# Kernel optimization log

Hardware: AMD Instinct MI355X
Metric: run time of the kernel (lower is better)

Reference implementation:

```python
import jax, jax.numpy as jnp
import numpy as np

N_NODES = 50000
N_EDGES = 800000
N_GRAPHS = 64
HID = 128
FEAT = 64
OUT = 32
N_LAYERS = 3
DECAY = 0.9
THRESH = 0.1


def setup_inputs() -> dict:
    key = jax.random.key(0)
    ks = jax.random.split(key, 24)
    s = 0.05
    inp = {
        "x": jax.random.normal(ks[0], (N_NODES, FEAT), jnp.float32),
        "edge_attr": jax.random.normal(ks[1], (N_EDGES, 1), jnp.float32),
        "initial_importance": jax.random.uniform(ks[2], (N_NODES, 1), jnp.float32),
        "imp_proj_W": jax.random.normal(ks[3], (1, HID), jnp.float32) * s,
        "imp_proj_b": jnp.zeros((HID,), jnp.float32),
        "init_W": jax.random.normal(ks[4], (FEAT + HID, HID), jnp.float32) * s,
        "init_b": jnp.zeros((HID,), jnp.float32),
        "msg_W": jax.random.normal(ks[5], (N_LAYERS, HID, HID), jnp.float32) * s,
        "msg_b": jnp.zeros((N_LAYERS, HID), jnp.float32),
        "upd_W": jax.random.normal(ks[6], (N_LAYERS, 2 * HID, HID), jnp.float32) * s,
        "upd_b": jnp.zeros((N_LAYERS, HID), jnp.float32),
        "gate_W": jax.random.normal(ks[7], (N_LAYERS, HID + 1, HID), jnp.float32) * s,
        "gate_b": jnp.zeros((N_LAYERS, HID), jnp.float32),
        "prop_W": jax.random.normal(ks[8], (N_LAYERS, HID, 1), jnp.float32) * s,
        "prop_b": jnp.zeros((N_LAYERS, 1), jnp.float32),
        "norm_w": jnp.ones((N_LAYERS, HID), jnp.float32),
        "norm_b": jnp.zeros((N_LAYERS, HID), jnp.float32),
        "norm_a": jnp.ones((N_LAYERS, HID), jnp.float32),
        "final_W": jax.random.normal(ks[9], (HID, OUT), jnp.float32) * s,
        "final_b": jnp.zeros((OUT,), jnp.float32),
        "edge_index": jax.random.randint(ks[10], (2, N_EDGES), 0, N_NODES, jnp.int32),
        # evenly spread sorted graph ids -> every graph non-empty
        "batch": (jnp.arange(N_NODES, dtype=jnp.int32) * N_GRAPHS) // N_NODES,
    }
    return inp


def _normalize_importance(imp, batch):
    # per-graph min/max normalization, fused segment reductions
    mn = jax.ops.segment_min(imp, batch, num_segments=N_GRAPHS)[batch]
    mx = jax.ops.segment_max(imp, batch, num_segments=N_GRAPHS)[batch]
    return (imp - mn) / (mx - mn + 1e-8)


def _graph_norm(x, batch, counts, w, b, a):
    # PyG GraphNorm: y = w * (x - a*mean) / sqrt(var(x - a*mean) + eps) + b
    mean = jax.ops.segment_sum(x, batch, num_segments=N_GRAPHS) / counts
    out = x - a * mean[batch]
    var = jax.ops.segment_sum(out * out, batch, num_segments=N_GRAPHS) / counts
    std = jnp.sqrt(var + 1e-5)
    return w * out / std[batch] + b


def _forward(x, edge_attr, initial_importance, imp_proj_W, imp_proj_b, init_W,
             init_b, msg_W, msg_b, upd_W, upd_b, gate_W, gate_b, prop_W, prop_b,
             norm_w, norm_b, norm_a, final_W, final_b, edge_index, batch):
    src, dst = edge_index[0], edge_index[1]
    counts = jax.ops.segment_sum(jnp.ones((N_NODES, 1), x.dtype), batch,
                                 num_segments=N_GRAPHS)  # [G,1]

    imp0 = initial_importance[:, 0]                       # [N]
    importance = _normalize_importance(imp0, batch)       # [N]
    imp_emb = importance[:, None] @ imp_proj_W + imp_proj_b  # [N,H]
    h = jnp.concatenate([x, imp_emb], axis=-1) @ init_W + init_b  # [N,H]

    for l in range(N_LAYERS):
        # MPNN: gather -> linear -> scatter-add -> update
        msg = h[src] @ msg_W[l] + msg_b[l]                # [E,H]
        aggr = jax.ops.segment_sum(msg, dst, num_segments=N_NODES)  # [N,H]
        conv = jnp.concatenate([h, aggr], axis=-1) @ upd_W[l] + upd_b[l]
        # importance gating
        gate_in = jnp.concatenate([conv, importance[:, None]], axis=-1)
        gate = jax.nn.sigmoid(gate_in @ gate_W[l] + gate_b[l])
        out = gate * conv + (1.0 - gate) * h
        prop = out @ prop_W[l] + prop_b[l]                # [N,1]
        # norm + relu (dropout p=0 in eval)
        h = jax.nn.relu(_graph_norm(out, batch, counts, norm_w[l], norm_b[l], norm_a[l]))
        # importance update
        imp = DECAY * importance + (1.0 - DECAY) * prop[:, 0]
        imp = _normalize_importance(imp, batch)
        imp = jnp.where(imp < THRESH, 0.0, imp)
        importance = _normalize_importance(imp, batch)

    h = h @ final_W + final_b                             # [N,OUT]
    logits = jax.ops.segment_sum(h, batch, num_segments=N_GRAPHS) / counts  # [G,OUT]
    final_importance = _normalize_importance(imp0 + importance, batch)
    return logits, final_importance[:, None]


def reference(x, edge_attr, initial_importance, imp_proj_W, imp_proj_b, init_W,
              init_b, msg_W, msg_b, upd_W, upd_b, gate_W, gate_b, prop_W, prop_b,
              norm_w, norm_b, norm_a, final_W, final_b, edge_index, batch):
    return _forward(x, edge_attr, initial_importance, imp_proj_W, imp_proj_b,
                    init_W, init_b, msg_W, msg_b, upd_W, upd_b, gate_W, gate_b,
                    prop_W, prop_b, norm_w, norm_b, norm_a, final_W, final_b,
                    edge_index, batch)
```

## Files before the change

kernel.cpp:

```cpp
#include <hip/hip_runtime.h>
#include <cstdint>

#define NN 50000
#define NE 800000
#define NG 64
#define HD 128
#define FT 64
#define NLAYERS 3
#define MB 32
#define NBLK 1563

__global__ void k_gbounds(const int* __restrict__ batch, int* __restrict__ gstart){
    int i = blockIdx.x*blockDim.x + threadIdx.x;
    if (i >= NN) return;
    int g = batch[i];
    if (i == 0){ for (int q = 0; q <= g; ++q) gstart[q] = 0; }
    else { int gp = batch[i-1]; for (int q = gp+1; q <= g; ++q) gstart[q] = i; }
    if (i == NN-1){ for (int q = g+1; q <= NG; ++q) gstart[q] = NN; }
}

__device__ __forceinline__ void block_minmax(float lmn, float lmx, float* red,
                                             float& omn, float& omx){
    #pragma unroll
    for (int off = 32; off > 0; off >>= 1){
        lmn = fminf(lmn, __shfl_xor(lmn, off));
        lmx = fmaxf(lmx, __shfl_xor(lmx, off));
    }
    int wave = threadIdx.x >> 6;
    if ((threadIdx.x & 63) == 0){ red[wave] = lmn; red[4+wave] = lmx; }
    __syncthreads();
    omn = fminf(fminf(red[0], red[1]), fminf(red[2], red[3]));
    omx = fmaxf(fmaxf(red[4], red[5]), fmaxf(red[6], red[7]));
    __syncthreads();
}

__global__ __launch_bounds__(256) void k_norm_graph(
    const float* __restrict__ va, const int* __restrict__ gstart,
    float* __restrict__ out)
{
    __shared__ float sv[1024];
    __shared__ float red[8];
    int g = blockIdx.x;
    int s = gstart[g], n = gstart[g+1] - s;
    int tid = threadIdx.x;
    float lmn = 3.4e38f, lmx = -3.4e38f;
    for (int i = tid; i < n; i += 256){
        float v = va[s+i];
        sv[i] = v;
        lmn = fminf(lmn, v); lmx = fmaxf(lmx, v);
    }
    float lo, hi;
    block_minmax(lmn, lmx, red, lo, hi);
    float inv = 1.f/(hi - lo + 1e-8f);
    for (int i = tid; i < n; i += 256) out[s+i] = (sv[i] - lo)*inv;
}

__global__ void k_fold_init(const float* __restrict__ pW, const float* __restrict__ pb,
                            const float* __restrict__ iW, const float* __restrict__ ib,
                            float* __restrict__ W0, float* __restrict__ b0){
    int j = threadIdx.x;
    for (int k = 0; k < FT; ++k) W0[k*HD + j] = iW[k*HD + j];
    float w2 = 0.f, b2 = 0.f;
    for (int k = 0; k < HD; ++k){
        float w = iW[(FT + k)*HD + j];
        w2 += pW[k]*w;
        b2 += pb[k]*w;
    }
    W0[FT*HD + j] = w2;
    b0[j] = ib[j] + b2;
}

__global__ void k_fold_layer(const float* __restrict__ msgW, const float* __restrict__ updW,
                             const float* __restrict__ msgb,
                             float* __restrict__ WfA, float* __restrict__ bcvA){
    int l = blockIdx.y;
    const float* mW  = msgW + (size_t)l*HD*HD;
    const float* uW  = updW + (size_t)l*2*HD*HD;
    const float* mb  = msgb + (size_t)l*HD;
    float* Wf  = WfA  + (size_t)l*2*HD*HD;
    float* bcv = bcvA + (size_t)l*HD;
    int j = threadIdx.x;
    int r = blockIdx.x;
    if (r < HD){
        Wf[(size_t)r*HD + j] = uW[(size_t)r*HD + j];
    } else if (r < 2*HD){
        int rr = r - HD;
        const float* uWbot = uW + (size_t)HD*HD;
        float acc = 0.f;
        for (int k = 0; k < HD; ++k)
            acc = fmaf(mW[(size_t)rr*HD + k], uWbot[(size_t)k*HD + j], acc);
        Wf[(size_t)r*HD + j] = acc;
    } else {
        const float* uWbot = uW + (size_t)HD*HD;
        float acc = 0.f;
        for (int k = 0; k < HD; ++k)
            acc = fmaf(mb[k], uWbot[(size_t)k*HD + j], acc);
        bcv[j] = acc;
    }
}

__global__ __launch_bounds__(256) void k_init(
    const float* __restrict__ x, const float* __restrict__ imp,
    const float* __restrict__ W0, const float* __restrict__ b0v,
    float* __restrict__ h)
{
    __shared__ float lds[MB][FT];
    __shared__ float scs[MB];
    int base = blockIdx.x*MB, tid = threadIdx.x;
    #pragma unroll
    for (int i = 0; i < 2; ++i){
        int fidx = i*256 + tid;
        int t = fidx >> 4, c = fidx & 15;
        float4 v = {0.f,0.f,0.f,0.f};
        if (base + t < NN) v = *(const float4*)&x[(size_t)(base+t)*FT + c*4];
        *(float4*)&lds[t][c*4] = v;
    }
    if (tid < MB) scs[tid] = (base+tid < NN) ? imp[base+tid] : 0.f;
    __syncthreads();

    const int cg = tid & 31, rg = tid >> 5;
    const int c0 = cg*4, r0 = rg*4;
    const float4 wl4 = *(const float4*)&W0[(size_t)FT*HD + c0];
    const float4 b4  = *(const float4*)&b0v[c0];
    float acc[4][4];
    #pragma unroll
    for (int r = 0; r < 4; ++r){
        float s = scs[r0+r];
        acc[r][0] = fmaf(s, wl4.x, b4.x); acc[r][1] = fmaf(s, wl4.y, b4.y);
        acc[r][2] = fmaf(s, wl4.z, b4.z); acc[r][3] = fmaf(s, wl4.w, b4.w);
    }
    for (int k4 = 0; k4 < 16; ++k4){
        const float4 w0 = *(const float4*)&W0[(size_t)(k4*4+0)*HD + c0];
        const float4 w1 = *(const float4*)&W0[(size_t)(k4*4+1)*HD + c0];
        const float4 w2 = *(const float4*)&W0[(size_t)(k4*4+2)*HD + c0];
        const float4 w3 = *(const float4*)&W0[(size_t)(k4*4+3)*HD + c0];
        #pragma unroll
        for (int r = 0; r < 4; ++r){
            const float4 a = *(const float4*)&lds[r0+r][k4*4];
            acc[r][0]=fmaf(a.x,w0.x,fmaf(a.y,w1.x,fmaf(a.z,w2.x,fmaf(a.w,w3.x,acc[r][0]))));
            acc[r][1]=fmaf(a.x,w0.y,fmaf(a.y,w1.y,fmaf(a.z,w2.y,fmaf(a.w,w3.y,acc[r][1]))));
            acc[r][2]=fmaf(a.x,w0.z,fmaf(a.y,w1.z,fmaf(a.z,w2.z,fmaf(a.w,w3.z,acc[r][2]))));
            acc[r][3]=fmaf(a.x,w0.w,fmaf(a.y,w1.w,fmaf(a.z,w2.w,fmaf(a.w,w3.w,acc[r][3]))));
        }
    }
    #pragma unroll
    for (int r = 0; r < 4; ++r)
        if (base + r0 + r < NN)
            *(float4*)&h[(size_t)(base+r0+r)*HD + c0] =
                make_float4(acc[r][0], acc[r][1], acc[r][2], acc[r][3]);
}

__global__ __launch_bounds__(256) void k_layer(
    const float* __restrict__ h, const float* __restrict__ aggr,
    const float* __restrict__ imp, const int* __restrict__ deg,
    const float* __restrict__ Wf, const float* __restrict__ bcv,
    const float* __restrict__ ub,
    const float* __restrict__ gW, const float* __restrict__ gb,
    const float* __restrict__ prW, const float* __restrict__ prb,
    float* __restrict__ outbuf, float* __restrict__ ta)
{
    __shared__ float lds[MB][256];
    __shared__ float clds[MB][HD];
    __shared__ float scs[MB];
    __shared__ float dgs[MB];
    __shared__ float red[8][4];
    const int base = blockIdx.x*MB, tid = threadIdx.x;

    #pragma unroll
    for (int i = 0; i < 8; ++i){
        int fidx = i*256 + tid;
        int t = fidx >> 6, c = fidx & 63;
        float4 v = {0.f,0.f,0.f,0.f};
        if (base + t < NN){
            const float* srcp = (c < 32) ? &h[(size_t)(base+t)*HD + c*4]
                                         : &aggr[(size_t)(base+t)*HD + (c-32)*4];
            v = *(const float4*)srcp;
        }
        *(float4*)&lds[t][c*4] = v;
    }
    if (tid < MB) scs[tid] = (base+tid < NN) ? imp[base+tid] : 0.f;
    else if (tid < 2*MB){
        int t = tid - MB;
        dgs[t] = (base+t < NN) ? (float)deg[base+t] : 0.f;
    }
    __syncthreads();

    const int cg = tid & 31, rg = tid >> 5;
    const int c0 = cg*4, r0 = rg*4;

    const float4 bc4 = *(const float4*)&bcv[c0];
    const float4 ub4 = *(const float4*)&ub[c0];
    float acc[4][4];
    #pragma unroll
    for (int r = 0; r < 4; ++r){
        float d = dgs[r0+r];
        acc[r][0] = fmaf(d, bc4.x, ub4.x); acc[r][1] = fmaf(d, bc4.y, ub4.y);
        acc[r][2] = fmaf(d, bc4.z, ub4.z); acc[r][3] = fmaf(d, bc4.w, ub4.w);
    }
    for (int k4 = 0; k4 < 64; ++k4){
        const float4 w0 = *(const float4*)&Wf[(size_t)(k4*4+0)*HD + c0];
        const float4 w1 = *(const float4*)&Wf[(size_t)(k4*4+1)*HD + c0];
        const float4 w2 = *(const float4*)&Wf[(size_t)(k4*4+2)*HD + c0];
        const float4 w3 = *(const float4*)&Wf[(size_t)(k4*4+3)*HD + c0];
        #pragma unroll
        for (int r = 0; r < 4; ++r){
            const float4 a = *(const float4*)&lds[r0+r][k4*4];
            acc[r][0]=fmaf(a.x,w0.x,fmaf(a.y,w1.x,fmaf(a.z,w2.x,fmaf(a.w,w3.x,acc[r][0]))));
            acc[r][1]=fmaf(a.x,w0.y,fmaf(a.y,w1.y,fmaf(a.z,w2.y,fmaf(a.w,w3.y,acc[r][1]))));
            acc[r][2]=fmaf(a.x,w0.z,fmaf(a.y,w1.z,fmaf(a.z,w2.z,fmaf(a.w,w3.z,acc[r][2]))));
            acc[r][3]=fmaf(a.x,w0.w,fmaf(a.y,w1.w,fmaf(a.z,w2.w,fmaf(a.w,w3.w,acc[r][3]))));
        }
    }
    #pragma unroll
    for (int r = 0; r < 4; ++r)
        *(float4*)&clds[r0+r][c0] = make_float4(acc[r][0],acc[r][1],acc[r][2],acc[r][3]);
    __syncthreads();

    const float4 gwl = *(const float4*)&gW[(size_t)HD*HD + c0];
    const float4 gb4 = *(const float4*)&gb[c0];
    float z[4][4];
    #pragma unroll
    for (int r = 0; r < 4; ++r){
        float s = scs[r0+r];
        z[r][0] = fmaf(s, gwl.x, gb4.x); z[r][1] = fmaf(s, gwl.y, gb4.y);
        z[r][2] = fmaf(s, gwl.z, gb4.z); z[r][3] = fmaf(s, gwl.w, gb4.w);
    }
    for (int k4 = 0; k4 < 32; ++k4){
        const float4 w0 = *(const float4*)&gW[(size_t)(k4*4+0)*HD + c0];
        const float4 w1 = *(const float4*)&gW[(size_t)(k4*4+1)*HD + c0];
        const float4 w2 = *(const float4*)&gW[(size_t)(k4*4+2)*HD + c0];
        const float4 w3 = *(const float4*)&gW[(size_t)(k4*4+3)*HD + c0];
        #pragma unroll
        for (int r = 0; r < 4; ++r){
            const float4 a = *(const float4*)&clds[r0+r][k4*4];
            z[r][0]=fmaf(a.x,w0.x,fmaf(a.y,w1.x,fmaf(a.z,w2.x,fmaf(a.w,w3.x,z[r][0]))));
            z[r][1]=fmaf(a.x,w0.y,fmaf(a.y,w1.y,fmaf(a.z,w2.y,fmaf(a.w,w3.y,z[r][1]))));
            z[r][2]=fmaf(a.x,w0.z,fmaf(a.y,w1.z,fmaf(a.z,w2.z,fmaf(a.w,w3.z,z[r][2]))));
            z[r][3]=fmaf(a.x,w0.w,fmaf(a.y,w1.w,fmaf(a.z,w2.w,fmaf(a.w,w3.w,z[r][3]))));
        }
    }

    const float4 pr4 = *(const float4*)&prW[c0];
    float psum[4];
    #pragma unroll
    for (int r = 0; r < 4; ++r){
        const float4 hv = *(const float4*)&lds[r0+r][c0];
        float g0 = 1.f/(1.f + expf(-z[r][0]));
        float g1 = 1.f/(1.f + expf(-z[r][1]));
        float g2 = 1.f/(1.f + expf(-z[r][2]));
        float g3 = 1.f/(1.f + expf(-z[r][3]));
        float o0 = g0*acc[r][0] + (1.f-g0)*hv.x;
        float o1 = g1*acc[r][1] + (1.f-g1)*hv.y;
        float o2 = g2*acc[r][2] + (1.f-g2)*hv.z;
        float o3 = g3*acc[r][3] + (1.f-g3)*hv.w;
        if (base + r0 + r < NN)
            *(float4*)&outbuf[(size_t)(base+r0+r)*HD + c0] = make_float4(o0,o1,o2,o3);
        psum[r] = o0*pr4.x + o1*pr4.y + o2*pr4.z + o3*pr4.w;
    }
    #pragma unroll
    for (int r = 0; r < 4; ++r){
        float v = psum[r];
        #pragma unroll
        for (int off = 16; off > 0; off >>= 1) v += __shfl_xor(v, off);
        if (cg == 0) red[rg][r] = v;
    }
    __syncthreads();
    if (tid < MB && base + tid < NN)
        ta[base+tid] = 0.9f*scs[tid] + 0.1f*(red[tid>>2][tid&3] + prb[0]);
}

__global__ void k_deg(const int* __restrict__ dst, int* deg){
    int e = blockIdx.x*blockDim.x + threadIdx.x;
    if (e < NE) atomicAdd(&deg[dst[e]], 1);
}

__global__ __launch_bounds__(1024) void k_scan(const int* __restrict__ deg,
                                               int* __restrict__ rowstart){
    __shared__ int wtot[16];
    __shared__ int woff[16];
    __shared__ int carry;
    int tid = threadIdx.x, lane = tid & 63, wv = tid >> 6;
    if (tid == 0) carry = 0;
    __syncthreads();
    for (int base = 0; base < NN; base += 1024){
        int i = base + tid;
        int v = (i < NN) ? deg[i] : 0;
        int x = v;
        #pragma unroll
        for (int off = 1; off < 64; off <<= 1){
            int y = __shfl_up(x, off);
            if (lane >= off) x += y;
        }
        if (lane == 63) wtot[wv] = x;
        __syncthreads();
        if (tid == 0){
            int a = carry;
            for (int w2 = 0; w2 < 16; ++w2){ woff[w2] = a; a += wtot[w2]; }
            carry = a;
        }
        __syncthreads();
        if (i < NN) rowstart[i] = woff[wv] + x - v;
    }
    __syncthreads();
    if (tid == 0) rowstart[NN] = carry;
}

__global__ void k_copy_int(const int* __restrict__ a, int* __restrict__ b, int n){
    int i = blockIdx.x*blockDim.x + threadIdx.x;
    if (i < n) b[i] = a[i];
}

__global__ void k_fill(const int* __restrict__ src, const int* __restrict__ dst,
                       int* cursor, int* __restrict__ csr){
    int e = blockIdx.x*blockDim.x + threadIdx.x;
    if (e < NE){
        int d = dst[e];
        int p = atomicAdd(&cursor[d], 1);
        csr[p] = src[e];
    }
}

__global__ __launch_bounds__(256) void k_aggregate(
    const float* __restrict__ hm, const int* __restrict__ rowstart,
    const int* __restrict__ csr, float* __restrict__ aggr)
{
    int node = blockIdx.x*8 + (threadIdx.x >> 5);
    int lane = threadIdx.x & 31;
    float4 a0 = {0.f,0.f,0.f,0.f}, a1 = a0, a2 = a0, a3 = a0;
    float4 a4 = a0, a5 = a0, a6 = a0, a7 = a0;
    int e0 = rowstart[node], e1 = rowstart[node+1];
    int e = e0;
    for (; e + 7 < e1; e += 8){
        int s0 = csr[e],   s1 = csr[e+1], s2 = csr[e+2], s3 = csr[e+3];
        int s4 = csr[e+4], s5 = csr[e+5], s6 = csr[e+6], s7 = csr[e+7];
        const float4 v0 = *(const float4*)&hm[(size_t)s0*HD + lane*4];
        const float4 v1 = *(const float4*)&hm[(size_t)s1*HD + lane*4];
        const float4 v2 = *(const float4*)&hm[(size_t)s2*HD + lane*4];
        const float4 v3 = *(const float4*)&hm[(size_t)s3*HD + lane*4];
        const float4 v4 = *(const float4*)&hm[(size_t)s4*HD + lane*4];
        const float4 v5 = *(const float4*)&hm[(size_t)s5*HD + lane*4];
        const float4 v6 = *(const float4*)&hm[(size_t)s6*HD + lane*4];
        const float4 v7 = *(const float4*)&hm[(size_t)s7*HD + lane*4];
        a0.x += v0.x; a0.y += v0.y; a0.z += v0.z; a0.w += v0.w;
        a1.x += v1.x; a1.y += v1.y; a1.z += v1.z; a1.w += v1.w;
        a2.x += v2.x; a2.y += v2.y; a2.z += v2.z; a2.w += v2.w;
        a3.x += v3.x; a3.y += v3.y; a3.z += v3.z; a3.w += v3.w;
        a4.x += v4.x; a4.y += v4.y; a4.z += v4.z; a4.w += v4.w;
        a5.x += v5.x; a5.y += v5.y; a5.z += v5.z; a5.w += v5.w;
        a6.x += v6.x; a6.y += v6.y; a6.z += v6.z; a6.w += v6.w;
        a7.x += v7.x; a7.y += v7.y; a7.z += v7.z; a7.w += v7.w;
    }
    for (; e + 3 < e1; e += 4){
        int s0 = csr[e], s1 = csr[e+1], s2 = csr[e+2], s3 = csr[e+3];
        const float4 v0 = *(const float4*)&hm[(size_t)s0*HD + lane*4];
        const float4 v1 = *(const float4*)&hm[(size_t)s1*HD + lane*4];
        const float4 v2 = *(const float4*)&hm[(size_t)s2*HD + lane*4];
        const float4 v3 = *(const float4*)&hm[(size_t)s3*HD + lane*4];
        a0.x += v0.x; a0.y += v0.y; a0.z += v0.z; a0.w += v0.w;
        a1.x += v1.x; a1.y += v1.y; a1.z += v1.z; a1.w += v1.w;
        a2.x += v2.x; a2.y += v2.y; a2.z += v2.z; a2.w += v2.w;
        a3.x += v3.x; a3.y += v3.y; a3.z += v3.z; a3.w += v3.w;
    }
    for (; e < e1; ++e){
        int s0 = csr[e];
        const float4 v0 = *(const float4*)&hm[(size_t)s0*HD + lane*4];
        a0.x += v0.x; a0.y += v0.y; a0.z += v0.z; a0.w += v0.w;
    }
    a0.x += a1.x; a0.y += a1.y; a0.z += a1.z; a0.w += a1.w;
    a2.x += a3.x; a2.y += a3.y; a2.z += a3.z; a2.w += a3.w;
    a4.x += a5.x; a4.y += a5.y; a4.z += a5.z; a4.w += a5.w;
    a6.x += a7.x; a6.y += a7.y; a6.z += a7.z; a6.w += a7.w;
    a0.x += a2.x; a0.y += a2.y; a0.z += a2.z; a0.w += a2.w;
    a4.x += a6.x; a4.y += a6.y; a4.z += a6.z; a4.w += a6.w;
    a0.x += a4.x; a0.y += a4.y; a0.z += a4.z; a0.w += a4.w;
    *(float4*)&aggr[(size_t)node*HD + lane*4] = a0;
}

__global__ __launch_bounds__(256) void k_gnorm(
    const float* __restrict__ v, const int* __restrict__ gstart,
    const float* __restrict__ nw, const float* __restrict__ nb,
    const float* __restrict__ na, float* __restrict__ hout,
    const float* __restrict__ tsrc, float* __restrict__ tdst)
{
    int g = blockIdx.x;
    int part = blockIdx.y;
    int s = gstart[g], n = gstart[g+1] - s;
    int tid = threadIdx.x;

    if (part == 4){
        __shared__ float sv[1024];
        __shared__ float red[8];
        float lmn = 3.4e38f, lmx = -3.4e38f;
        for (int i = tid; i < n; i += 256){
            float val = tsrc[s+i]; sv[i] = val;
            lmn = fminf(lmn, val); lmx = fmaxf(lmx, val);
        }
        float lo, hi;
        block_minmax(lmn, lmx, red, lo, hi);
        float inv = 1.f/(hi - lo + 1e-8f);
        lmn = 3.4e38f; lmx = -3.4e38f;
        for (int i = tid; i < n; i += 256){
            float t2 = (sv[i] - lo)*inv;
            if (t2 < 0.1f) t2 = 0.f;
            sv[i] = t2;
            lmn = fminf(lmn, t2); lmx = fmaxf(lmx, t2);
        }
        float lo2, hi2;
        block_minmax(lmn, lmx, red, lo2, hi2);
        float inv2 = 1.f/(hi2 - lo2 + 1e-8f);
        for (int i = tid; i < n; i += 256) tdst[s+i] = (sv[i] - lo2)*inv2;
        return;
    }

    __shared__ float4 rs1[32][8];
    __shared__ float4 rs2[32][8];
    __shared__ float amv[32], scv[32], nbv[32];
    int rg = tid >> 3, c4l = tid & 7;
    size_t coff = (size_t)part*32 + c4l*4;
    float4 s1 = {0.f,0.f,0.f,0.f}, s2 = {0.f,0.f,0.f,0.f};
    for (int i = rg; i < n; i += 32){
        const float4 vv = *(const float4*)&v[(size_t)(s+i)*HD + coff];
        s1.x += vv.x; s1.y += vv.y; s1.z += vv.z; s1.w += vv.w;
        s2.x += vv.x*vv.x; s2.y += vv.y*vv.y; s2.z += vv.z*vv.z; s2.w += vv.w*vv.w;
    }
    rs1[rg][c4l] = s1; rs2[rg][c4l] = s2;
    __syncthreads();
    if (tid < 8){
        float4 t1 = {0.f,0.f,0.f,0.f}, t2 = {0.f,0.f,0.f,0.f};
        for (int r = 0; r < 32; ++r){
            float4 a = rs1[r][tid]; float4 b = rs2[r][tid];
            t1.x += a.x; t1.y += a.y; t1.z += a.z; t1.w += a.w;
            t2.x += b.x; t2.y += b.y; t2.z += b.z; t2.w += b.w;
        }
        float fn = (float)n;
        float S1[4] = {t1.x,t1.y,t1.z,t1.w};
        float S2[4] = {t2.x,t2.y,t2.z,t2.w};
        #pragma unroll
        for (int e = 0; e < 4; ++e){
            int j = part*32 + tid*4 + e;
            float m = S1[e]/fn;
            float aj = na[j];
            float var = S2[e]/fn - (2.f*aj - aj*aj)*m*m;
            float stdv = sqrtf(var + 1e-5f);
            amv[tid*4+e] = aj*m;
            scv[tid*4+e] = nw[j]/stdv;
            nbv[tid*4+e] = nb[j];
        }
    }
    __syncthreads();
    const float4 am4 = *(const float4*)&amv[c4l*4];
    const float4 sc4 = *(const float4*)&scv[c4l*4];
    const float4 nb4 = *(const float4*)&nbv[c4l*4];
    for (int i = rg; i < n; i += 32){
        const float4 vv = *(const float4*)&v[(size_t)(s+i)*HD + coff];
        float4 r;
        r.x = fmaxf((vv.x - am4.x)*sc4.x + nb4.x, 0.f);
        r.y = fmaxf((vv.y - am4.y)*sc4.y + nb4.y, 0.f);
        r.z = fmaxf((vv.z - am4.z)*sc4.z + nb4.z, 0.f);
        r.w = fmaxf((vv.w - am4.w)*sc4.w + nb4.w, 0.f);
        *(float4*)&hout[(size_t)(s+i)*HD + coff] = r;
    }
}

__global__ __launch_bounds__(1024) void k_logits(
    const float* __restrict__ h, const int* __restrict__ gstart,
    const float* __restrict__ fW, const float* __restrict__ fb,
    const float* __restrict__ imp0, const float* __restrict__ impf,
    float* __restrict__ outp)
{
    __shared__ float4 rs1[32][32];
    __shared__ float gsum[HD];
    __shared__ float redn[32];
    int g = blockIdx.x;
    int s = gstart[g], n = gstart[g+1] - s;
    int tid = threadIdx.x;
    int c4 = tid & 31, rg = tid >> 5;
    float4 s1 = {0.f,0.f,0.f,0.f};
    for (int i = rg; i < n; i += 32){
        const float4 vv = *(const float4*)&h[(size_t)(s+i)*HD + c4*4];
        s1.x += vv.x; s1.y += vv.y; s1.z += vv.z; s1.w += vv.w;
    }
    rs1[rg][c4] = s1;
    __syncthreads();
    if (tid < 32){
        float4 t1 = {0.f,0.f,0.f,0.f};
        for (int r = 0; r < 32; ++r){
            float4 a = rs1[r][tid];
            t1.x += a.x; t1.y += a.y; t1.z += a.z; t1.w += a.w;
        }
        gsum[tid*4+0] = t1.x; gsum[tid*4+1] = t1.y;
        gsum[tid*4+2] = t1.z; gsum[tid*4+3] = t1.w;
    }
    __syncthreads();
    if (tid < 32){
        int o = tid;
        float acc = 0.f;
        for (int k = 0; k < HD; ++k) acc = fmaf(gsum[k], fW[k*32 + o], acc);
        outp[g*32 + o] = acc/(float)n + fb[o];
    }
    float val = 0.f;
    bool has = (tid < n);
    float lmn = 3.4e38f, lmx = -3.4e38f;
    if (has){ val = imp0[s+tid] + impf[s+tid]; lmn = val; lmx = val; }
    #pragma unroll
    for (int off = 32; off > 0; off >>= 1){
        lmn = fminf(lmn, __shfl_xor(lmn, off));
        lmx = fmaxf(lmx, __shfl_xor(lmx, off));
    }
    int wv = tid >> 6, lane = tid & 63;
    if (lane == 0){ redn[wv] = lmn; redn[16+wv] = lmx; }
    __syncthreads();
    float lo = redn[0], hi = redn[16];
    for (int r2 = 1; r2 < 16; ++r2){
        lo = fminf(lo, redn[r2]); hi = fmaxf(hi, redn[16+r2]);
    }
    if (has) outp[NG*32 + s + tid] = (val - lo)/(hi - lo + 1e-8f);
}

extern "C" void kernel_launch(void* const* d_in, const int* in_sizes, int n_in,
                              void* d_out, int out_size, void* d_ws, size_t ws_size,
                              hipStream_t stream){
    const float* x    = (const float*)d_in[0];
    const float* imp0 = (const float*)d_in[2];
    const float* pW   = (const float*)d_in[3];
    const float* pb   = (const float*)d_in[4];
    const float* iW   = (const float*)d_in[5];
    const float* ib   = (const float*)d_in[6];
    const float* msgW = (const float*)d_in[7];
    const float* msgb = (const float*)d_in[8];
    const float* updW = (const float*)d_in[9];
    const float* updb = (const float*)d_in[10];
    const float* gWt  = (const float*)d_in[11];
    const float* gb   = (const float*)d_in[12];
    const float* prW  = (const float*)d_in[13];
    const float* prb  = (const float*)d_in[14];
    const float* nw   = (const float*)d_in[15];
    const float* nb   = (const float*)d_in[16];
    const float* na   = (const float*)d_in[17];
    const float* fW   = (const float*)d_in[18];
    const float* fb   = (const float*)d_in[19];
    const int* eidx   = (const int*)d_in[20];
    const int* batch  = (const int*)d_in[21];
    const int* esrc = eidx;
    const int* edst = eidx + NE;
    float* outp = (float*)d_out;

    char* w = (char*)d_ws;
    size_t off = 0;
    auto alloc = [&](size_t bytes)->char*{
        char* p = w + off;
        off += (bytes + 255) & ~(size_t)255;
        return p;
    };
    float* h     = (float*)alloc((size_t)NN*HD*4);
    float* aggB  = (float*)alloc((size_t)NN*HD*4);
    float* outA  = (float*)alloc((size_t)NN*HD*4);
    float* ta    = (float*)alloc((size_t)NN*4);
    float* imp   = (float*)alloc((size_t)NN*4);
    float* W0    = (float*)alloc((size_t)(FT+1)*HD*4);
    float* b0    = (float*)alloc((size_t)HD*4);
    float* Wf    = (float*)alloc((size_t)NLAYERS*2*HD*HD*4);
    float* bcv   = (float*)alloc((size_t)NLAYERS*HD*4);
    int* gstart  = (int*)alloc((size_t)(NG+1)*4);
    int* deg     = (int*)alloc((size_t)NN*4);
    int* rowst   = (int*)alloc((size_t)(NN+1)*4);
    int* cursor  = (int*)alloc((size_t)NN*4);
    int* csr     = (int*)alloc((size_t)NE*4);

    k_gbounds<<<196, 256, 0, stream>>>(batch, gstart);

    hipMemsetAsync(deg, 0, NN*4, stream);
    k_deg<<<3125, 256, 0, stream>>>(edst, deg);
    k_scan<<<1, 1024, 0, stream>>>(deg, rowst);
    k_copy_int<<<196, 256, 0, stream>>>(rowst, cursor, NN);
    k_fill<<<3125, 256, 0, stream>>>(esrc, edst, cursor, csr);

    k_fold_init<<<1, 128, 0, stream>>>(pW, pb, iW, ib, W0, b0);
    k_fold_layer<<<dim3(257, NLAYERS), 128, 0, stream>>>(msgW, updW, msgb, Wf, bcv);

    k_norm_graph<<<NG, 256, 0, stream>>>(imp0, gstart, imp);
    k_init<<<NBLK, 256, 0, stream>>>(x, imp, W0, b0, h);

    for (int l = 0; l < NLAYERS; ++l){
        k_aggregate<<<6250, 256, 0, stream>>>(h, rowst, csr, aggB);
        k_layer<<<NBLK, 256, 0, stream>>>(
            h, aggB, imp, deg,
            Wf + (size_t)l*2*HD*HD, bcv + (size_t)l*HD,
            updb + (size_t)l*HD, gWt + (size_t)l*(HD+1)*HD, gb + (size_t)l*HD,
            prW + (size_t)l*HD, prb + l, outA, ta);
        k_gnorm<<<dim3(NG,5), 256, 0, stream>>>(outA, gstart,
            nw + (size_t)l*HD, nb + (size_t)l*HD, na + (size_t)l*HD, h, ta, imp);
    }

    k_logits<<<NG, 1024, 0, stream>>>(h, gstart, fW, fb, imp0, imp, outp);
}
```

Measured before the change: 705.7 us.

## Split aggregation into feature slices with 4 lanes per node; trim layer LDS

The gather aggregation now splits the 128-wide feature row into 8 slices of 16 floats, one slice per block, with 4 threads per node and 64 nodes per block. Each block touches only a 64-byte column band of the node table, which is meant to shrink the working set each block pulls through cache. In exchange every block rereads the CSR row indices, about 8 times more index traffic overall. k_layer drops its separate clds buffer and reuses the upper half of lds after an extra barrier to cut LDS use, and it sets launch_bounds occupancy to 4 and adds unroll-4 pragmas on the GEMM loops.

```diff
diff --git a/kernel.cpp b/kernel.cpp
--- a/kernel.cpp
+++ b/kernel.cpp
@@ -9,6 +9,8 @@
 #define NLAYERS 3
 #define MB 32
 #define NBLK 1563
+#define AGN 64
+#define AGB (8*((NN + AGN - 1)/AGN))
 
 __global__ void k_gbounds(const int* __restrict__ batch, int* __restrict__ gstart){
     int i = blockIdx.x*blockDim.x + threadIdx.x;
@@ -129,6 +131,7 @@
         acc[r][0] = fmaf(s, wl4.x, b4.x); acc[r][1] = fmaf(s, wl4.y, b4.y);
         acc[r][2] = fmaf(s, wl4.z, b4.z); acc[r][3] = fmaf(s, wl4.w, b4.w);
     }
+    #pragma unroll 4
     for (int k4 = 0; k4 < 16; ++k4){
         const float4 w0 = *(const float4*)&W0[(size_t)(k4*4+0)*HD + c0];
         const float4 w1 = *(const float4*)&W0[(size_t)(k4*4+1)*HD + c0];
@@ -150,7 +153,7 @@
                 make_float4(acc[r][0], acc[r][1], acc[r][2], acc[r][3]);
 }
 
-__global__ __launch_bounds__(256) void k_layer(
+__global__ __launch_bounds__(256, 4) void k_layer(
     const float* __restrict__ h, const float* __restrict__ aggr,
     const float* __restrict__ imp, const int* __restrict__ deg,
     const float* __restrict__ Wf, const float* __restrict__ bcv,
@@ -160,7 +163,6 @@
     float* __restrict__ outbuf, float* __restrict__ ta)
 {
     __shared__ float lds[MB][256];
-    __shared__ float clds[MB][HD];
     __shared__ float scs[MB];
     __shared__ float dgs[MB];
     __shared__ float red[8][4];
@@ -197,6 +199,7 @@
         acc[r][0] = fmaf(d, bc4.x, ub4.x); acc[r][1] = fmaf(d, bc4.y, ub4.y);
         acc[r][2] = fmaf(d, bc4.z, ub4.z); acc[r][3] = fmaf(d, bc4.w, ub4.w);
     }
+    #pragma unroll 4
     for (int k4 = 0; k4 < 64; ++k4){
         const float4 w0 = *(const float4*)&Wf[(size_t)(k4*4+0)*HD + c0];
         const float4 w1 = *(const float4*)&Wf[(size_t)(k4*4+1)*HD + c0];
@@ -211,9 +214,10 @@
             acc[r][3]=fmaf(a.x,w0.w,fmaf(a.y,w1.w,fmaf(a.z,w2.w,fmaf(a.w,w3.w,acc[r][3]))));
         }
     }
+    __syncthreads();
     #pragma unroll
     for (int r = 0; r < 4; ++r)
-        *(float4*)&clds[r0+r][c0] = make_float4(acc[r][0],acc[r][1],acc[r][2],acc[r][3]);
+        *(float4*)&lds[r0+r][HD + c0] = make_float4(acc[r][0],acc[r][1],acc[r][2],acc[r][3]);
     __syncthreads();
 
     const float4 gwl = *(const float4*)&gW[(size_t)HD*HD + c0];
@@ -225,6 +229,7 @@
         z[r][0] = fmaf(s, gwl.x, gb4.x); z[r][1] = fmaf(s, gwl.y, gb4.y);
         z[r][2] = fmaf(s, gwl.z, gb4.z); z[r][3] = fmaf(s, gwl.w, gb4.w);
     }
+    #pragma unroll 4
     for (int k4 = 0; k4 < 32; ++k4){
         const float4 w0 = *(const float4*)&gW[(size_t)(k4*4+0)*HD + c0];
         const float4 w1 = *(const float4*)&gW[(size_t)(k4*4+1)*HD + c0];
@@ -232,7 +237,7 @@
         const float4 w3 = *(const float4*)&gW[(size_t)(k4*4+3)*HD + c0];
         #pragma unroll
         for (int r = 0; r < 4; ++r){
-            const float4 a = *(const float4*)&clds[r0+r][k4*4];
+            const float4 a = *(const float4*)&lds[r0+r][HD + k4*4];
             z[r][0]=fmaf(a.x,w0.x,fmaf(a.y,w1.x,fmaf(a.z,w2.x,fmaf(a.w,w3.x,z[r][0]))));
             z[r][1]=fmaf(a.x,w0.y,fmaf(a.y,w1.y,fmaf(a.z,w2.y,fmaf(a.w,w3.y,z[r][1]))));
             z[r][2]=fmaf(a.x,w0.z,fmaf(a.y,w1.z,fmaf(a.z,w2.z,fmaf(a.w,w3.z,z[r][2]))));
@@ -324,8 +329,13 @@
     const float* __restrict__ hm, const int* __restrict__ rowstart,
     const int* __restrict__ csr, float* __restrict__ aggr)
 {
-    int node = blockIdx.x*8 + (threadIdx.x >> 5);
-    int lane = threadIdx.x & 31;
+    int bid = blockIdx.x;
+    int slice = bid & 7;
+    int nb = bid >> 3;
+    int node = nb*AGN + (threadIdx.x >> 2);
+    if (node >= NN) return;
+    int ln = threadIdx.x & 3;
+    const float* __restrict__ hp = hm + (size_t)slice*16 + (size_t)ln*4;
     float4 a0 = {0.f,0.f,0.f,0.f}, a1 = a0, a2 = a0, a3 = a0;
     float4 a4 = a0, a5 = a0, a6 = a0, a7 = a0;
     int e0 = rowstart[node], e1 = rowstart[node+1];
@@ -333,14 +343,14 @@
     for (; e + 7 < e1; e += 8){
         int s0 = csr[e],   s1 = csr[e+1], s2 = csr[e+2], s3 = csr[e+3];
         int s4 = csr[e+4], s5 = csr[e+5], s6 = csr[e+6], s7 = csr[e+7];
-        const float4 v0 = *(const float4*)&hm[(size_t)s0*HD + lane*4];
-        const float4 v1 = *(const float4*)&hm[(size_t)s1*HD + lane*4];
-        const float4 v2 = *(const float4*)&hm[(size_t)s2*HD + lane*4];
-        const float4 v3 = *(const float4*)&hm[(size_t)s3*HD + lane*4];
-        const float4 v4 = *(const float4*)&hm[(size_t)s4*HD + lane*4];
-        const float4 v5 = *(const float4*)&hm[(size_t)s5*HD + lane*4];
-        const float4 v6 = *(const float4*)&hm[(size_t)s6*HD + lane*4];
-        const float4 v7 = *(const float4*)&hm[(size_t)s7*HD + lane*4];
+        const float4 v0 = *(const float4*)&hp[(size_t)s0*HD];
+        const float4 v1 = *(const float4*)&hp[(size_t)s1*HD];
+        const float4 v2 = *(const float4*)&hp[(size_t)s2*HD];
+        const float4 v3 = *(const float4*)&hp[(size_t)s3*HD];
+        const float4 v4 = *(const float4*)&hp[(size_t)s4*HD];
+        const float4 v5 = *(const float4*)&hp[(size_t)s5*HD];
+        const float4 v6 = *(const float4*)&hp[(size_t)s6*HD];
+        const float4 v7 = *(const float4*)&hp[(size_t)s7*HD];
         a0.x += v0.x; a0.y += v0.y; a0.z += v0.z; a0.w += v0.w;
         a1.x += v1.x; a1.y += v1.y; a1.z += v1.z; a1.w += v1.w;
         a2.x += v2.x; a2.y += v2.y; a2.z += v2.z; a2.w += v2.w;
@@ -352,10 +362,10 @@
     }
     for (; e + 3 < e1; e += 4){
         int s0 = csr[e], s1 = csr[e+1], s2 = csr[e+2], s3 = csr[e+3];
-        const float4 v0 = *(const float4*)&hm[(size_t)s0*HD + lane*4];
-        const float4 v1 = *(const float4*)&hm[(size_t)s1*HD + lane*4];
-        const float4 v2 = *(const float4*)&hm[(size_t)s2*HD + lane*4];
-        const float4 v3 = *(const float4*)&hm[(size_t)s3*HD + lane*4];
+        const float4 v0 = *(const float4*)&hp[(size_t)s0*HD];
+        const float4 v1 = *(const float4*)&hp[(size_t)s1*HD];
+        const float4 v2 = *(const float4*)&hp[(size_t)s2*HD];
+        const float4 v3 = *(const float4*)&hp[(size_t)s3*HD];
         a0.x += v0.x; a0.y += v0.y; a0.z += v0.z; a0.w += v0.w;
         a1.x += v1.x; a1.y += v1.y; a1.z += v1.z; a1.w += v1.w;
         a2.x += v2.x; a2.y += v2.y; a2.z += v2.z; a2.w += v2.w;
@@ -363,7 +373,7 @@
     }
     for (; e < e1; ++e){
         int s0 = csr[e];
-        const float4 v0 = *(const float4*)&hm[(size_t)s0*HD + lane*4];
+        const float4 v0 = *(const float4*)&hp[(size_t)s0*HD];
         a0.x += v0.x; a0.y += v0.y; a0.z += v0.z; a0.w += v0.w;
     }
     a0.x += a1.x; a0.y += a1.y; a0.z += a1.z; a0.w += a1.w;
@@ -373,7 +383,7 @@
     a0.x += a2.x; a0.y += a2.y; a0.z += a2.z; a0.w += a2.w;
     a4.x += a6.x; a4.y += a6.y; a4.z += a6.z; a4.w += a6.w;
     a0.x += a4.x; a0.y += a4.y; a0.z += a4.z; a0.w += a4.w;
-    *(float4*)&aggr[(size_t)node*HD + lane*4] = a0;
+    *(float4*)&aggr[(size_t)node*HD + slice*16 + ln*4] = a0;
 }
 
 __global__ __launch_bounds__(256) void k_gnorm(
@@ -582,7 +592,7 @@
     k_init<<<NBLK, 256, 0, stream>>>(x, imp, W0, b0, h);
 
     for (int l = 0; l < NLAYERS; ++l){
-        k_aggregate<<<6250, 256, 0, stream>>>(h, rowst, csr, aggB);
+        k_aggregate<<<AGB, 256, 0, stream>>>(h, rowst, csr, aggB);
         k_layer<<<NBLK, 256, 0, stream>>>(
             h, aggB, imp, deg,
             Wf + (size_t)l*2*HD*HD, bcv + (size_t)l*HD,
```

Result: slower. 763.1 us (+8.1%).
